# Optimization experiments

Hardware: AMD Instinct MI355X
Metric: run time of the kernel (lower is better)

The kernel has to match this reference:

```python
import jax, jax.numpy as jnp
import numpy as np

H = 1024
N_IDX = 400000
NBINS = 256


def setup_inputs() -> dict:
    key = jax.random.key(0)
    ks = jax.random.split(key, 10)
    return {
        "input_data": jax.random.uniform(ks[0], (1, 3, H, H), jnp.float32),
        "target_data": jax.random.uniform(ks[1], (1, 3, H, H), jnp.float32) * 2.0 - 1.0,
        "ref": jax.random.uniform(ks[2], (1, 3, H, H), jnp.float32) * 2.0 - 1.0,
        "mask_src": (jax.random.uniform(ks[3], (1, 1, H, H)) > 0.3).astype(jnp.float32) * 255.0,
        "mask_tar": (jax.random.uniform(ks[4], (1, 1, H, H)) > 0.3).astype(jnp.float32) * 255.0,
        "target_data_eye": jax.random.uniform(ks[5], (1, 3, H, H), jnp.float32),
        "idx0": jax.random.randint(ks[6], (N_IDX,), 0, H),
        "idx1": jax.random.randint(ks[7], (N_IDX,), 0, H),
        "idx2": jax.random.randint(ks[8], (N_IDX,), 0, H),
        "idx3": jax.random.randint(ks[9], (N_IDX,), 0, H),
    }


def _cdf(vals):
    # vals: [3, N] float in [0, 256). torch.histc(bins=256, min=0, max=256) -> bin = floor(v)
    bins = jnp.clip(vals.astype(jnp.int32), 0, NBINS - 1)  # [3, N]
    hist = jnp.zeros((3, NBINS), jnp.float32).at[jnp.arange(3)[:, None], bins].add(1.0)
    cdf = jnp.cumsum(hist, axis=1)
    return cdf / cdf[:, -1:]  # normalized cumulative histogram, [3, 256]


def _trans_table(cdf_dst, cdf_ref):
    # cal_trans(ref=cdf_dst, adj=cdf_ref): table[i] = first j in [1,255]
    # with cdf_ref[j-1] <= cdf_dst[i] <= cdf_ref[j]; else table[i] = i; table[255] = 255
    r = cdf_dst[:, None]                  # [256, 1]
    lo = cdf_ref[None, :-1]               # [1, 255] -> adj[j-1], j = 1..255
    hi = cdf_ref[None, 1:]                # [1, 255] -> adj[j]
    cond = (r >= lo) & (r <= hi)          # [256, 255]
    has = cond.any(axis=1)
    j = jnp.argmax(cond, axis=1) + 1      # first matching j
    table = jnp.where(has, j, jnp.arange(NBINS))
    return table.at[NBINS - 1].set(NBINS - 1)


def _hist_match(dst_img, ref_img, i0, i1, i2, i3):
    # dst_img, ref_img: [3, H, W]; gather masked pixels per channel
    dst_align = dst_img[:, i0, i1]        # [3, N]
    ref_align = ref_img[:, i2, i3]        # [3, N]
    cdf_dst = _cdf(dst_align)
    cdf_ref = _cdf(ref_align)
    tables = jax.vmap(_trans_table)(cdf_dst, cdf_ref)  # [3, 256] int
    bins = jnp.clip(dst_align.astype(jnp.int32), 0, NBINS - 1)  # int() truncation, v >= 0
    matched = jnp.take_along_axis(tables, bins, axis=1).astype(dst_img.dtype)  # [3, N]
    return dst_img.at[:, i0, i1].set(matched)


def reference(input_data, target_data, ref, mask_src, mask_tar, target_data_eye,
              idx0, idx1, idx2, idx3):
    # part = 'lip' (generic part) -> histogram_matching branch; use_vgg = False
    de_norm = lambda x: jnp.clip((x + 1.0) / 2.0, 0.0, 1.0)
    target = (de_norm(target_data) * 255.0)[0]          # [3, H, W]
    inp = (jnp.clip(input_data, 0.0, 1.0) * 255.0)[0]   # [3, H, W]
    r = (de_norm(ref) * 255.0)[0]                       # [3, H, W]
    msrc = jnp.broadcast_to(mask_src / 255.0, (1, 3, H, H))[0]
    mtar = jnp.broadcast_to(mask_tar / 255.0, (1, 3, H, H))[0]

    input_masked = inp * msrc
    target_masked = target * mtar
    ref_masked = r * msrc

    input_match = jax.lax.stop_gradient(
        _hist_match(ref_masked, target_masked, idx0, idx1, idx2, idx3))

    loss = jnp.mean(jnp.abs(input_masked / 255.0 - input_match / 255.0))
    return ((target_masked / 255.0)[None], (ref_masked / 255.0)[None],
            (input_masked / 255.0)[None], (input_match / 255.0)[None], loss)
```

## Files before the change

### kernel.cpp

```cpp
#include <hip/hip_runtime.h>

#define H 1024
#define HH (H * H)
#define CHW (3 * HH)
#define NB 256
#define HIST_BLOCKS 768
#define FIN_BLOCKS 512

__device__ __forceinline__ float clamp01(float x) { return fminf(fmaxf(x, 0.0f), 1.0f); }

__device__ __forceinline__ unsigned int bin8(float v01) {
    int b = (int)(v01 * 255.0f);
    return (unsigned int)min(max(b, 0), NB - 1);
}

__global__ void k_elementwise(const float4* __restrict__ inp,
                              const float4* __restrict__ tar,
                              const float4* __restrict__ rfp,
                              const float4* __restrict__ msrc,
                              const float4* __restrict__ mtar,
                              float4* __restrict__ out0, float4* __restrict__ out1,
                              float4* __restrict__ out2,
                              uint4* __restrict__ pk_dst, uint4* __restrict__ pk_ref,
                              unsigned int* __restrict__ gz,
                              unsigned int* __restrict__ bm,
                              float* __restrict__ loss)
{
    if (blockIdx.x == 0) {
        for (int i = threadIdx.x; i < 1536; i += blockDim.x) gz[i] = 0u;
        if (threadIdx.x == 0) *loss = 0.0f;
    } else if (blockIdx.x <= 32) {
        int base = (int)(blockIdx.x - 1) * 1024;
        for (int i = threadIdx.x; i < 1024; i += blockDim.x) bm[base + i] = 0u;
    }
    int p = blockIdx.x * blockDim.x + threadIdx.x;
    if (p >= HH / 4) return;
    float4 ms4 = msrc[p], mt4 = mtar[p];
    float msx = ms4.x / 255.0f, msy = ms4.y / 255.0f, msz = ms4.z / 255.0f, msw = ms4.w / 255.0f;
    float mtx = mt4.x / 255.0f, mty = mt4.y / 255.0f, mtz = mt4.z / 255.0f, mtw = mt4.w / 255.0f;
    unsigned int bd0 = 0, bd1 = 0, bd2 = 0, bd3 = 0;
    unsigned int br0 = 0, br1 = 0, br2 = 0, br3 = 0;
#pragma unroll
    for (int c = 0; c < 3; ++c) {
        int q = c * (HH / 4) + p;
        float4 t = tar[q], r = rfp[q], iv = inp[q];
        float4 o0, o1, o2;
        o0.x = clamp01((t.x + 1.0f) * 0.5f) * mtx;
        o0.y = clamp01((t.y + 1.0f) * 0.5f) * mty;
        o0.z = clamp01((t.z + 1.0f) * 0.5f) * mtz;
        o0.w = clamp01((t.w + 1.0f) * 0.5f) * mtw;
        o1.x = clamp01((r.x + 1.0f) * 0.5f) * msx;
        o1.y = clamp01((r.y + 1.0f) * 0.5f) * msy;
        o1.z = clamp01((r.z + 1.0f) * 0.5f) * msz;
        o1.w = clamp01((r.w + 1.0f) * 0.5f) * msw;
        o2.x = clamp01(iv.x) * msx;
        o2.y = clamp01(iv.y) * msy;
        o2.z = clamp01(iv.z) * msz;
        o2.w = clamp01(iv.w) * msw;
        out0[q] = o0;
        out1[q] = o1;
        out2[q] = o2;
        int sh = 8 * c;
        bd0 |= bin8(o1.x) << sh;  bd1 |= bin8(o1.y) << sh;
        bd2 |= bin8(o1.z) << sh;  bd3 |= bin8(o1.w) << sh;
        br0 |= bin8(o0.x) << sh;  br1 |= bin8(o0.y) << sh;
        br2 |= bin8(o0.z) << sh;  br3 |= bin8(o0.w) << sh;
    }
    pk_dst[p] = make_uint4(bd0, bd1, bd2, bd3);
    pk_ref[p] = make_uint4(br0, br1, br2, br3);
}

__global__ void k_hist(const unsigned int* __restrict__ pk_dst,
                       const unsigned int* __restrict__ pk_ref,
                       const int* __restrict__ i0, const int* __restrict__ i1,
                       const int* __restrict__ i2, const int* __restrict__ i3,
                       unsigned int* __restrict__ ghist,
                       unsigned int* __restrict__ bm, int n)
{
    __shared__ unsigned int h[2 * 3 * NB];
    for (int i = threadIdx.x; i < 2 * 3 * NB; i += blockDim.x) h[i] = 0u;
    __syncthreads();

    int lane = threadIdx.x & 63;
    for (int k = blockIdx.x * blockDim.x + threadIdx.x; k < n; k += gridDim.x * blockDim.x) {
        int pd = i0[k] * H + i1[k];
        int pr = i2[k] * H + i3[k];
        unsigned int a = pk_dst[pd];
        unsigned int b = pk_ref[pr];

        atomicOr(&bm[(unsigned int)pd >> 5], 1u << (pd & 31));

        unsigned long long mza = __ballot(a == 0u);
        if (a != 0u) {
            atomicAdd(&h[        (a       & 255u)], 1u);
            atomicAdd(&h[  NB + ((a >> 8) & 255u)], 1u);
            atomicAdd(&h[2*NB + ((a >>16) & 255u)], 1u);
        } else if (lane == __ffsll(mza) - 1) {
            unsigned int cnt = (unsigned int)__popcll(mza);
            atomicAdd(&h[0],      cnt);
            atomicAdd(&h[NB],     cnt);
            atomicAdd(&h[2 * NB], cnt);
        }

        unsigned long long mzb = __ballot(b == 0u);
        if (b != 0u) {
            atomicAdd(&h[3*NB + ( b       & 255u)], 1u);
            atomicAdd(&h[4*NB + ((b >> 8) & 255u)], 1u);
            atomicAdd(&h[5*NB + ((b >>16) & 255u)], 1u);
        } else if (lane == __ffsll(mzb) - 1) {
            unsigned int cnt = (unsigned int)__popcll(mzb);
            atomicAdd(&h[3 * NB], cnt);
            atomicAdd(&h[4 * NB], cnt);
            atomicAdd(&h[5 * NB], cnt);
        }
    }
    __syncthreads();
    for (int i = threadIdx.x; i < 2 * 3 * NB; i += blockDim.x) {
        unsigned int v = h[i];
        if (v) atomicAdd(&ghist[i], v);
    }
}

__global__ __launch_bounds__(384)
void k_finalize(const uint4* __restrict__ ghist4,
                const unsigned int* __restrict__ bm,
                const float4* __restrict__ out1v,
                const float4* __restrict__ out2v,
                float4* __restrict__ out3v,
                float* __restrict__ loss)
{
    __shared__ float cdf[6][NB];
    __shared__ float tl[3 * NB];
    __shared__ float ws[6];
    int t = threadIdx.x;
    int wave = t >> 6, lane = t & 63;

    uint4 v = ghist4[wave * 64 + lane];
    unsigned int s0 = v.x;
    unsigned int s1 = s0 + v.y;
    unsigned int s2 = s1 + v.z;
    unsigned int s3 = s2 + v.w;

    unsigned int scan = s3;
#pragma unroll
    for (int off = 1; off < 64; off <<= 1) {
        unsigned int u = (unsigned int)__shfl_up((int)scan, off, 64);
        if (lane >= off) scan += u;
    }
    unsigned int prefix = scan - s3;
    unsigned int total  = (unsigned int)__shfl((int)scan, 63, 64);
    float ft = (float)total;

    cdf[wave][lane * 4 + 0] = (float)(prefix + s0) / ft;
    cdf[wave][lane * 4 + 1] = (float)(prefix + s1) / ft;
    cdf[wave][lane * 4 + 2] = (float)(prefix + s2) / ft;
    cdf[wave][lane * 4 + 3] = (float)(prefix + s3) / ft;
    __syncthreads();

    if (t < NB) {
#pragma unroll
        for (int c = 0; c < 3; ++c) {
            float r = cdf[c][t];
            const float* cr = cdf[3 + c];
            int lo = 1, hi = NB - 1;
#pragma unroll
            for (int it = 0; it < 8; ++it) {
                int mid = (lo + hi) >> 1;
                if (cr[mid] >= r) hi = mid; else lo = mid + 1;
            }
            int jstar = lo - 1;
            int tab = (jstar == 0 && cr[0] > r) ? t : (jstar + 1);
            if (t == NB - 1) tab = NB - 1;
            tl[c * NB + t] = (float)tab / 255.0f;
        }
    }
    __syncthreads();

    float s = 0.0f;
    const int n4 = HH / 4;
    for (int k = blockIdx.x * blockDim.x + t; k < n4; k += gridDim.x * blockDim.x) {
        unsigned int w = bm[k >> 3];
        unsigned int nib = (w >> ((k & 7) * 4)) & 0xFu;
#pragma unroll
        for (int c = 0; c < 3; ++c) {
            float4 a = out1v[c * n4 + k];
            float4 b = out2v[c * n4 + k];
            float4 o;
            o.x = (nib & 1u) ? tl[c * NB + bin8(a.x)] : a.x;
            o.y = (nib & 2u) ? tl[c * NB + bin8(a.y)] : a.y;
            o.z = (nib & 4u) ? tl[c * NB + bin8(a.z)] : a.z;
            o.w = (nib & 8u) ? tl[c * NB + bin8(a.w)] : a.w;
            out3v[c * n4 + k] = o;
            s += fabsf(b.x - o.x) + fabsf(b.y - o.y) + fabsf(b.z - o.z) + fabsf(b.w - o.w);
        }
    }
#pragma unroll
    for (int off = 32; off > 0; off >>= 1) s += __shfl_down(s, off);
    if (lane == 0) ws[wave] = s;
    __syncthreads();
    if (t == 0) {
        float tsum = ws[0] + ws[1] + ws[2] + ws[3] + ws[4] + ws[5];
        atomicAdd(loss, tsum * (1.0f / (float)CHW));
    }
}

extern "C" void kernel_launch(void* const* d_in, const int* in_sizes, int n_in,
                              void* d_out, int out_size, void* d_ws, size_t ws_size,
                              hipStream_t stream)
{
    const float* inp  = (const float*)d_in[0];
    const float* tar  = (const float*)d_in[1];
    const float* rfp  = (const float*)d_in[2];
    const float* msrc = (const float*)d_in[3];
    const float* mtar = (const float*)d_in[4];
    const int* i0 = (const int*)d_in[6];
    const int* i1 = (const int*)d_in[7];
    const int* i2 = (const int*)d_in[8];
    const int* i3 = (const int*)d_in[9];
    int n = in_sizes[6];

    float* out0 = (float*)d_out;
    float* out1 = out0 + CHW;
    float* out2 = out1 + CHW;
    float* out3 = out2 + CHW;
    float* loss = out3 + CHW;

    unsigned int* ghist  = (unsigned int*)d_ws;
    unsigned int* bm     = (unsigned int*)((char*)d_ws + 8192);
    unsigned int* pk_dst = (unsigned int*)((char*)d_ws + 139264);
    unsigned int* pk_ref = pk_dst + HH;

    k_elementwise<<<(HH / 4 + 255) / 256, 256, 0, stream>>>(
        (const float4*)inp, (const float4*)tar, (const float4*)rfp,
        (const float4*)msrc, (const float4*)mtar,
        (float4*)out0, (float4*)out1, (float4*)out2,
        (uint4*)pk_dst, (uint4*)pk_ref, ghist, bm, loss);

    k_hist<<<HIST_BLOCKS, 512, 0, stream>>>(pk_dst, pk_ref, i0, i1, i2, i3, ghist, bm, n);

    k_finalize<<<FIN_BLOCKS, 384, 0, stream>>>(
        (const uint4*)ghist, bm, (const float4*)out1, (const float4*)out2,
        (float4*)out3, loss);
}
```

Baseline: 175.2 us.

## Count index multiplicities per pixel first, fuse histogram into elementwise pass

A new counting kernel scatters atomic increments into per-pixel 8-bit multiplicity counters for the gathered dst and ref indices. The elementwise kernel then builds the shared-memory histograms directly from its freshly computed bins, weighted by those counts. This removes the packed-bin intermediate buffers and the random gather of them in a separate histogram kernel. The finalize pass now reads the byte counters as its match mask instead of a bitmask. In exchange it adds a workspace memset and global atomics on the counters, and a pixel hit more than 255 times would overflow into its neighbour's byte.

```diff
diff --git a/kernel.cpp b/kernel.cpp
--- a/kernel.cpp
+++ b/kernel.cpp
@@ -4,7 +4,10 @@
 #define HH (H * H)
 #define CHW (3 * HH)
 #define NB 256
-#define HIST_BLOCKS 768
+#define NTHR 256
+#define NGR (HH / 4)
+#define NBLK (NGR / NTHR)
+#define CNT_BLOCKS 512
 #define FIN_BLOCKS 512
 
 __device__ __forceinline__ float clamp01(float x) { return fminf(fmaxf(x, 0.0f), 1.0f); }
@@ -14,45 +17,55 @@
     return (unsigned int)min(max(b, 0), NB - 1);
 }
 
-__global__ void k_elementwise(const float4* __restrict__ inp,
-                              const float4* __restrict__ tar,
-                              const float4* __restrict__ rfp,
-                              const float4* __restrict__ msrc,
-                              const float4* __restrict__ mtar,
-                              float4* __restrict__ out0, float4* __restrict__ out1,
-                              float4* __restrict__ out2,
-                              uint4* __restrict__ pk_dst, uint4* __restrict__ pk_ref,
-                              unsigned int* __restrict__ gz,
-                              unsigned int* __restrict__ bm,
-                              float* __restrict__ loss)
-{
-    if (blockIdx.x == 0) {
-        for (int i = threadIdx.x; i < 1536; i += blockDim.x) gz[i] = 0u;
-        if (threadIdx.x == 0) *loss = 0.0f;
-    } else if (blockIdx.x <= 32) {
-        int base = (int)(blockIdx.x - 1) * 1024;
-        for (int i = threadIdx.x; i < 1024; i += blockDim.x) bm[base + i] = 0u;
-    }
-    int p = blockIdx.x * blockDim.x + threadIdx.x;
-    if (p >= HH / 4) return;
+__global__ void k_count(const int* __restrict__ i0, const int* __restrict__ i1,
+                        const int* __restrict__ i2, const int* __restrict__ i3,
+                        unsigned int* __restrict__ cntd, unsigned int* __restrict__ cntr,
+                        float* __restrict__ loss, int n)
+{
+    if (blockIdx.x == 0 && threadIdx.x == 0) *loss = 0.0f;
+    int stride = gridDim.x * blockDim.x;
+    for (int k = blockIdx.x * blockDim.x + threadIdx.x; k < n; k += stride) {
+        int pd = i0[k] * H + i1[k];
+        int pr = i2[k] * H + i3[k];
+        atomicAdd(&cntd[pd >> 2], 1u << (8 * (pd & 3)));
+        atomicAdd(&cntr[pr >> 2], 1u << (8 * (pr & 3)));
+    }
+}
+
+__global__ __launch_bounds__(NTHR)
+void k_elementwise(const float4* __restrict__ inp, const float4* __restrict__ tar,
+                   const float4* __restrict__ rfp, const float4* __restrict__ msrc,
+                   const float4* __restrict__ mtar,
+                   float4* __restrict__ out0, float4* __restrict__ out1,
+                   float4* __restrict__ out2,
+                   const unsigned int* __restrict__ cntd,
+                   const unsigned int* __restrict__ cntr,
+                   unsigned int* __restrict__ ghist)
+{
+    __shared__ unsigned int h[6 * NB];
+    for (int i = threadIdx.x; i < 6 * NB; i += NTHR) h[i] = 0u;
+    __syncthreads();
+
+    const int p = blockIdx.x * NTHR + threadIdx.x;
+
     float4 ms4 = msrc[p], mt4 = mtar[p];
     float msx = ms4.x / 255.0f, msy = ms4.y / 255.0f, msz = ms4.z / 255.0f, msw = ms4.w / 255.0f;
     float mtx = mt4.x / 255.0f, mty = mt4.y / 255.0f, mtz = mt4.z / 255.0f, mtw = mt4.w / 255.0f;
-    unsigned int bd0 = 0, bd1 = 0, bd2 = 0, bd3 = 0;
-    unsigned int br0 = 0, br1 = 0, br2 = 0, br3 = 0;
+    unsigned int bd[4] = {0u, 0u, 0u, 0u};
+    unsigned int br[4] = {0u, 0u, 0u, 0u};
 #pragma unroll
     for (int c = 0; c < 3; ++c) {
-        int q = c * (HH / 4) + p;
-        float4 t = tar[q], r = rfp[q], iv = inp[q];
+        int q = c * NGR + p;
+        float4 tv = tar[q], rv = rfp[q], iv = inp[q];
         float4 o0, o1, o2;
-        o0.x = clamp01((t.x + 1.0f) * 0.5f) * mtx;
-        o0.y = clamp01((t.y + 1.0f) * 0.5f) * mty;
-        o0.z = clamp01((t.z + 1.0f) * 0.5f) * mtz;
-        o0.w = clamp01((t.w + 1.0f) * 0.5f) * mtw;
-        o1.x = clamp01((r.x + 1.0f) * 0.5f) * msx;
-        o1.y = clamp01((r.y + 1.0f) * 0.5f) * msy;
-        o1.z = clamp01((r.z + 1.0f) * 0.5f) * msz;
-        o1.w = clamp01((r.w + 1.0f) * 0.5f) * msw;
+        o0.x = clamp01((tv.x + 1.0f) * 0.5f) * mtx;
+        o0.y = clamp01((tv.y + 1.0f) * 0.5f) * mty;
+        o0.z = clamp01((tv.z + 1.0f) * 0.5f) * mtz;
+        o0.w = clamp01((tv.w + 1.0f) * 0.5f) * mtw;
+        o1.x = clamp01((rv.x + 1.0f) * 0.5f) * msx;
+        o1.y = clamp01((rv.y + 1.0f) * 0.5f) * msy;
+        o1.z = clamp01((rv.z + 1.0f) * 0.5f) * msz;
+        o1.w = clamp01((rv.w + 1.0f) * 0.5f) * msw;
         o2.x = clamp01(iv.x) * msx;
         o2.y = clamp01(iv.y) * msy;
         o2.z = clamp01(iv.z) * msz;
@@ -61,61 +74,32 @@
         out1[q] = o1;
         out2[q] = o2;
         int sh = 8 * c;
-        bd0 |= bin8(o1.x) << sh;  bd1 |= bin8(o1.y) << sh;
-        bd2 |= bin8(o1.z) << sh;  bd3 |= bin8(o1.w) << sh;
-        br0 |= bin8(o0.x) << sh;  br1 |= bin8(o0.y) << sh;
-        br2 |= bin8(o0.z) << sh;  br3 |= bin8(o0.w) << sh;
-    }
-    pk_dst[p] = make_uint4(bd0, bd1, bd2, bd3);
-    pk_ref[p] = make_uint4(br0, br1, br2, br3);
-}
-
-__global__ void k_hist(const unsigned int* __restrict__ pk_dst,
-                       const unsigned int* __restrict__ pk_ref,
-                       const int* __restrict__ i0, const int* __restrict__ i1,
-                       const int* __restrict__ i2, const int* __restrict__ i3,
-                       unsigned int* __restrict__ ghist,
-                       unsigned int* __restrict__ bm, int n)
-{
-    __shared__ unsigned int h[2 * 3 * NB];
-    for (int i = threadIdx.x; i < 2 * 3 * NB; i += blockDim.x) h[i] = 0u;
-    __syncthreads();
-
-    int lane = threadIdx.x & 63;
-    for (int k = blockIdx.x * blockDim.x + threadIdx.x; k < n; k += gridDim.x * blockDim.x) {
-        int pd = i0[k] * H + i1[k];
-        int pr = i2[k] * H + i3[k];
-        unsigned int a = pk_dst[pd];
-        unsigned int b = pk_ref[pr];
-
-        atomicOr(&bm[(unsigned int)pd >> 5], 1u << (pd & 31));
-
-        unsigned long long mza = __ballot(a == 0u);
-        if (a != 0u) {
-            atomicAdd(&h[        (a       & 255u)], 1u);
-            atomicAdd(&h[  NB + ((a >> 8) & 255u)], 1u);
-            atomicAdd(&h[2*NB + ((a >>16) & 255u)], 1u);
-        } else if (lane == __ffsll(mza) - 1) {
-            unsigned int cnt = (unsigned int)__popcll(mza);
-            atomicAdd(&h[0],      cnt);
-            atomicAdd(&h[NB],     cnt);
-            atomicAdd(&h[2 * NB], cnt);
-        }
-
-        unsigned long long mzb = __ballot(b == 0u);
-        if (b != 0u) {
-            atomicAdd(&h[3*NB + ( b       & 255u)], 1u);
-            atomicAdd(&h[4*NB + ((b >> 8) & 255u)], 1u);
-            atomicAdd(&h[5*NB + ((b >>16) & 255u)], 1u);
-        } else if (lane == __ffsll(mzb) - 1) {
-            unsigned int cnt = (unsigned int)__popcll(mzb);
-            atomicAdd(&h[3 * NB], cnt);
-            atomicAdd(&h[4 * NB], cnt);
-            atomicAdd(&h[5 * NB], cnt);
-        }
-    }
-    __syncthreads();
-    for (int i = threadIdx.x; i < 2 * 3 * NB; i += blockDim.x) {
+        bd[0] |= bin8(o1.x) << sh;  bd[1] |= bin8(o1.y) << sh;
+        bd[2] |= bin8(o1.z) << sh;  bd[3] |= bin8(o1.w) << sh;
+        br[0] |= bin8(o0.x) << sh;  br[1] |= bin8(o0.y) << sh;
+        br[2] |= bin8(o0.z) << sh;  br[3] |= bin8(o0.w) << sh;
+    }
+
+    unsigned int wd = cntd[p], wr = cntr[p];
+#pragma unroll
+    for (int j = 0; j < 4; ++j) {
+        unsigned int wj = (wd >> (8 * j)) & 255u;
+        if (wj) {
+            unsigned int b = bd[j];
+            atomicAdd(&h[        (b        & 255u)], wj);
+            atomicAdd(&h[  NB + ((b >>  8) & 255u)], wj);
+            atomicAdd(&h[2*NB + ((b >> 16) & 255u)], wj);
+        }
+        unsigned int vj = (wr >> (8 * j)) & 255u;
+        if (vj) {
+            unsigned int b = br[j];
+            atomicAdd(&h[3*NB + ( b        & 255u)], vj);
+            atomicAdd(&h[4*NB + ((b >>  8) & 255u)], vj);
+            atomicAdd(&h[5*NB + ((b >> 16) & 255u)], vj);
+        }
+    }
+    __syncthreads();
+    for (int i = threadIdx.x; i < 6 * NB; i += NTHR) {
         unsigned int v = h[i];
         if (v) atomicAdd(&ghist[i], v);
     }
@@ -123,7 +107,7 @@
 
 __global__ __launch_bounds__(384)
 void k_finalize(const uint4* __restrict__ ghist4,
-                const unsigned int* __restrict__ bm,
+                const unsigned int* __restrict__ cntd,
                 const float4* __restrict__ out1v,
                 const float4* __restrict__ out2v,
                 float4* __restrict__ out3v,
@@ -179,17 +163,16 @@
     float s = 0.0f;
     const int n4 = HH / 4;
     for (int k = blockIdx.x * blockDim.x + t; k < n4; k += gridDim.x * blockDim.x) {
-        unsigned int w = bm[k >> 3];
-        unsigned int nib = (w >> ((k & 7) * 4)) & 0xFu;
+        unsigned int w = cntd[k];
 #pragma unroll
         for (int c = 0; c < 3; ++c) {
             float4 a = out1v[c * n4 + k];
             float4 b = out2v[c * n4 + k];
             float4 o;
-            o.x = (nib & 1u) ? tl[c * NB + bin8(a.x)] : a.x;
-            o.y = (nib & 2u) ? tl[c * NB + bin8(a.y)] : a.y;
-            o.z = (nib & 4u) ? tl[c * NB + bin8(a.z)] : a.z;
-            o.w = (nib & 8u) ? tl[c * NB + bin8(a.w)] : a.w;
+            o.x = ( w        & 255u) ? tl[c * NB + bin8(a.x)] : a.x;
+            o.y = ((w >>  8) & 255u) ? tl[c * NB + bin8(a.y)] : a.y;
+            o.z = ((w >> 16) & 255u) ? tl[c * NB + bin8(a.z)] : a.z;
+            o.w = ( w >> 24        ) ? tl[c * NB + bin8(a.w)] : a.w;
             out3v[c * n4 + k] = o;
             s += fabsf(b.x - o.x) + fabsf(b.y - o.y) + fabsf(b.z - o.z) + fabsf(b.w - o.w);
         }
@@ -225,20 +208,21 @@
     float* out3 = out2 + CHW;
     float* loss = out3 + CHW;
 
-    unsigned int* ghist  = (unsigned int*)d_ws;
-    unsigned int* bm     = (unsigned int*)((char*)d_ws + 8192);
-    unsigned int* pk_dst = (unsigned int*)((char*)d_ws + 139264);
-    unsigned int* pk_ref = pk_dst + HH;
-
-    k_elementwise<<<(HH / 4 + 255) / 256, 256, 0, stream>>>(
+    unsigned int* ghist = (unsigned int*)d_ws;
+    unsigned int* cntd  = (unsigned int*)((char*)d_ws + 8192);
+    unsigned int* cntr  = cntd + NGR;
+
+    hipMemsetAsync(d_ws, 0, 8192 + 2 * (size_t)NGR * 4, stream);
+
+    k_count<<<CNT_BLOCKS, 256, 0, stream>>>(i0, i1, i2, i3, cntd, cntr, loss, n);
+
+    k_elementwise<<<NBLK, NTHR, 0, stream>>>(
         (const float4*)inp, (const float4*)tar, (const float4*)rfp,
         (const float4*)msrc, (const float4*)mtar,
         (float4*)out0, (float4*)out1, (float4*)out2,
-        (uint4*)pk_dst, (uint4*)pk_ref, ghist, bm, loss);
-
-    k_hist<<<HIST_BLOCKS, 512, 0, stream>>>(pk_dst, pk_ref, i0, i1, i2, i3, ghist, bm, n);
+        cntd, cntr, ghist);
 
     k_finalize<<<FIN_BLOCKS, 384, 0, stream>>>(
-        (const uint4*)ghist, bm, (const float4*)out1, (const float4*)out2,
+        (const uint4*)ghist, cntd, (const float4*)out1, (const float4*)out2,
         (float4*)out3, loss);
 }
```

Result: slower. 182.2 us (+4.0%).
